# Optimization experiments

Measured on AMD Instinct MI355X. Metric: run time of the kernel, lower is better.

## Reference

```python
import jax, jax.numpy as jnp
import numpy as np

N_GOAL, N_OBS, N_TASK = 16384, 65536, 8192
E1, E2 = 1048576, 1048576
B = 256            # graphs in batch
F, S = 128, 64     # dim_features, dim_state


def setup_inputs() -> dict:
    key = jax.random.key(0)
    ks = jax.random.split(key, 16)
    inp = {
        "x_goal": jax.random.normal(ks[0], (N_GOAL, F), jnp.float32),
        "x_obs": jax.random.normal(ks[1], (N_OBS, F), jnp.float32),
        "x_task": jax.random.normal(ks[2], (N_TASK, S), jnp.float32),
        "ei_go_src": jax.random.randint(ks[3], (E1,), 0, N_GOAL),
        "ei_go_dst": jax.random.randint(ks[4], (E1,), 0, N_OBS),
        "ei_ot_src": jax.random.randint(ks[5], (E2,), 0, N_OBS),
        "ei_ot_dst": jax.random.randint(ks[6], (E2,), 0, N_TASK),
        # contiguous graph assignment: 32 task nodes per graph
        "task_batch": jnp.arange(N_TASK) // (N_TASK // B),
        # GinStandardMLP (state_gin): Lin(F,S)-ReLU-Lin(S,S)-ReLU
        "W1": jax.random.normal(ks[7], (F, S), jnp.float32) * 0.05,
        "b1": jnp.zeros((S,), jnp.float32),
        "W2": jax.random.normal(ks[8], (S, S), jnp.float32) * 0.05,
        "b2": jnp.zeros((S,), jnp.float32),
        # GinUnactivatedMLP (action_gin): Lin(S,S)-ReLU-Lin(S,1)
        "W3": jax.random.normal(ks[9], (S, S), jnp.float32) * 0.05,
        "b3": jnp.zeros((S,), jnp.float32),
        "W4": jax.random.normal(ks[10], (S, 1), jnp.float32) * 0.05,
        "b4": jnp.zeros((1,), jnp.float32),
        # critic head: Lin(2,8)-ReLU-Lin(8,1)
        "Wc1": jax.random.normal(ks[11], (2, 8), jnp.float32) * 0.5,
        "bc1": jnp.zeros((8,), jnp.float32),
        "Wc2": jax.random.normal(ks[12], (8, 1), jnp.float32) * 0.5,
        "bc2": jnp.zeros((1,), jnp.float32),
    }
    return inp


def reference(x_goal, x_obs, x_task,
              ei_go_src, ei_go_dst, ei_ot_src, ei_ot_dst, task_batch,
              W1, b1, W2, b2, W3, b3, W4, b4, Wc1, bc1, Wc2, bc2):
    # --- state_gin: GINConv((goal, obs)), eps=0 ---
    agg1 = jax.ops.segment_sum(x_goal[ei_go_src], ei_go_dst, num_segments=N_OBS)
    h = x_obs + agg1                              # (1+eps)*x_dst + sum_j x_src
    h = jax.nn.relu(h @ W1 + b1)
    x1 = jax.nn.relu(h @ W2 + b2)                 # [N_OBS, S]

    # --- action_gin: GINConv((obs, task)), eps=0 ---
    agg2 = jax.ops.segment_sum(x1[ei_ot_src], ei_ot_dst, num_segments=N_TASK)
    g = x_task + agg2
    g = jax.nn.relu(g @ W3 + b3)
    x2 = g @ W4 + b4                              # [N_TASK, 1]

    # --- critic path: global max / mean pool over task nodes per graph ---
    max_pool = jax.ops.segment_max(x2, task_batch, num_segments=B)   # [B, 1]
    cnt = jax.ops.segment_sum(jnp.ones((N_TASK, 1), x2.dtype), task_batch, num_segments=B)
    mean_pool = jax.ops.segment_sum(x2, task_batch, num_segments=B) / cnt  # [B, 1]

    pooled = jnp.concatenate([max_pool.max(axis=1, keepdims=True),
                              mean_pool.mean(axis=1, keepdims=True)], axis=1)  # [B, 2]
    out = jax.nn.relu(pooled @ Wc1 + bc1) @ Wc2 + bc2                 # [B, 1]
    return out.squeeze(-1)                                            # [B]
```

## Files before the change

### kernel.cpp

```cpp
#include <hip/hip_runtime.h>
#include <hip/hip_bf16.h>


#define CAP1 2816
#define CAP2 5120

__global__ __launch_bounds__(256) void gemm_all(
    const float* __restrict__ x_goal, const float* __restrict__ x_obs,
    const float* __restrict__ W, float* __restrict__ xg1,
    float* __restrict__ obs)
{
    __shared__ float Ws[128 * 64];
    __shared__ float Xs[16 * 132];
    const int tid = threadIdx.x;
    const float* X;
    float* O;
    int row0;
    if (blockIdx.x < 1024) { X = x_goal; O = xg1; row0 = blockIdx.x * 16; }
    else                   { X = x_obs;  O = obs; row0 = (blockIdx.x - 1024) * 16; }
    for (int i = tid; i < 128 * 64 / 4; i += 256)
        ((float4*)Ws)[i] = ((const float4*)W)[i];
    for (int i = tid; i < 16 * 32; i += 256) {
        int r = i >> 5, c4 = i & 31;
        float4 v = ((const float4*)(X + (size_t)(row0 + r) * 128))[c4];
        *((float4*)(Xs + r * 132 + c4 * 4)) = v;
    }
    __syncthreads();
    const int rl = tid >> 4;
    const int cg = (tid & 15) * 4;
    float a0 = 0.f, a1 = 0.f, a2 = 0.f, a3 = 0.f;
    const float* xr = Xs + rl * 132;
    #pragma unroll 8
    for (int k = 0; k < 128; ++k) {
        float xv = xr[k];
        float4 wv = *((const float4*)(Ws + k * 64 + cg));
        a0 = fmaf(xv, wv.x, a0);
        a1 = fmaf(xv, wv.y, a1);
        a2 = fmaf(xv, wv.z, a2);
        a3 = fmaf(xv, wv.w, a3);
    }
    float4 o; o.x = a0; o.y = a1; o.z = a2; o.w = a3;
    *((float4*)(O + (size_t)(row0 + rl) * 64 + cg)) = o;
}

__global__ __launch_bounds__(256) void bin_edges_all(
    const int* __restrict__ go_src, const int* __restrict__ go_dst,
    const int* __restrict__ ot_src, const int* __restrict__ ot_dst,
    int* __restrict__ gcur1, int* __restrict__ gcur2,
    int* __restrict__ pairs1, int* __restrict__ pairs2, int nblk1)
{
    __shared__ int hist[512];
    __shared__ int cur[512];
    const int tid = threadIdx.x;
    const bool s1 = (int)blockIdx.x < nblk1;
    const int* src = s1 ? go_src : ot_src;
    const int* dst = s1 ? go_dst : ot_dst;
    int* gcur  = s1 ? gcur1 : gcur2;
    int* pairs = s1 ? pairs1 : pairs2;
    const int bsh  = s1 ? 7 : 5;
    const int rowm = s1 ? 127 : 31;
    const int nb   = s1 ? 512 : 256;
    const int cap  = s1 ? CAP1 : CAP2;
    const int blk  = s1 ? blockIdx.x : blockIdx.x - nblk1;

    for (int i = tid; i < nb; i += 256) hist[i] = 0;
    __syncthreads();
    const int base = blk * 4096;
    const int4* d4 = (const int4*)(dst + base);
    const int4* s4 = (const int4*)(src + base);
    int4 dv[4];
    #pragma unroll
    for (int k = 0; k < 4; ++k) {
        dv[k] = d4[k * 256 + tid];
        atomicAdd(&hist[dv[k].x >> bsh], 1);
        atomicAdd(&hist[dv[k].y >> bsh], 1);
        atomicAdd(&hist[dv[k].z >> bsh], 1);
        atomicAdd(&hist[dv[k].w >> bsh], 1);
    }
    __syncthreads();
    for (int i = tid; i < nb; i += 256)
        cur[i] = atomicAdd(&gcur[i], hist[i]);
    __syncthreads();
    #pragma unroll
    for (int k = 0; k < 4; ++k) {
        int4 sv = s4[k * 256 + tid];
        int d, s, b, p;
        d = dv[k].x; s = sv.x; b = d >> bsh; p = atomicAdd(&cur[b], 1);
        if (p < cap) pairs[(size_t)b * cap + p] = ((d & rowm) << 17) | s;
        d = dv[k].y; s = sv.y; b = d >> bsh; p = atomicAdd(&cur[b], 1);
        if (p < cap) pairs[(size_t)b * cap + p] = ((d & rowm) << 17) | s;
        d = dv[k].z; s = sv.z; b = d >> bsh; p = atomicAdd(&cur[b], 1);
        if (p < cap) pairs[(size_t)b * cap + p] = ((d & rowm) << 17) | s;
        d = dv[k].w; s = sv.w; b = d >> bsh; p = atomicAdd(&cur[b], 1);
        if (p < cap) pairs[(size_t)b * cap + p] = ((d & rowm) << 17) | s;
    }
}

__global__ __launch_bounds__(1024) void gather_mlp_obs(
    const int* __restrict__ pairs, const int* __restrict__ cnt,
    const float* __restrict__ xg1, const float* __restrict__ obs,
    const float* __restrict__ b1, const float* __restrict__ W2,
    const float* __restrict__ b2, float* __restrict__ x1)
{
    constexpr int ROWS = 128;
    __shared__ int ssrc[CAP1];
    __shared__ int offs[ROWS + 1];
    __shared__ int rcnt[ROWS];
    __shared__ float W2t[64 * 68];
    __shared__ float hb[16 * 64];
    const int tid = threadIdx.x;
    const int b = blockIdx.x;

    #pragma unroll
    for (int i = tid; i < 4096; i += 1024) {
        int k = i >> 6, c = i & 63;
        W2t[c * 68 + k] = W2[i];
    }
    if (tid < ROWS) rcnt[tid] = 0;
    __syncthreads();
    int n = cnt[b];
    if (n > CAP1) n = CAP1;
    const int* bp = pairs + (size_t)b * CAP1;

    int e0 = -1, e1 = -1, e2 = -1;
    {
        int i = tid;
        if (i < n) {
            e0 = bp[i]; atomicAdd(&rcnt[e0 >> 17], 1); i += 1024;
            if (i < n) {
                e1 = bp[i]; atomicAdd(&rcnt[e1 >> 17], 1); i += 1024;
                if (i < n) { e2 = bp[i]; atomicAdd(&rcnt[e2 >> 17], 1); }
            }
        }
    }
    __syncthreads();
    if (tid < 64) {
        int v0 = rcnt[2 * tid], v1 = rcnt[2 * tid + 1];
        int s = v0 + v1;
        #pragma unroll
        for (int d = 1; d < 64; d <<= 1) {
            int t = __shfl_up(s, d);
            if (tid >= d) s += t;
        }
        int ex = s - v0 - v1;
        offs[2 * tid] = ex;
        offs[2 * tid + 1] = ex + v0;
        rcnt[2 * tid] = ex;
        rcnt[2 * tid + 1] = ex + v0;
        if (tid == 63) offs[ROWS] = s;
    }
    __syncthreads();
    if (e0 >= 0) { int p = atomicAdd(&rcnt[e0 >> 17], 1); ssrc[p] = e0 & 0x1FFFF; }
    if (e1 >= 0) { int p = atomicAdd(&rcnt[e1 >> 17], 1); ssrc[p] = e1 & 0x1FFFF; }
    if (e2 >= 0) { int p = atomicAdd(&rcnt[e2 >> 17], 1); ssrc[p] = e2 & 0x1FFFF; }
    __syncthreads();
    const int wv = tid >> 6;
    const int lane = tid & 63;
    const float bb1 = b1[lane];
    const float bb2 = b2[lane];
    float* hp = hb + wv * 64;
    const float4* h4 = (const float4*)hp;
    const float4* wrow = (const float4*)(W2t + lane * 68);
    for (int r = wv; r < ROWS; r += 16) {
        int beg = offs[r], end = offs[r + 1];
        float a0 = 0.f, a1 = 0.f, a2 = 0.f, a3 = 0.f;
        int e = beg;
        for (; e + 4 <= end; e += 4) {
            int s0 = ssrc[e], s1 = ssrc[e + 1], s2 = ssrc[e + 2], s3 = ssrc[e + 3];
            a0 += xg1[(size_t)s0 * 64 + lane];
            a1 += xg1[(size_t)s1 * 64 + lane];
            a2 += xg1[(size_t)s2 * 64 + lane];
            a3 += xg1[(size_t)s3 * 64 + lane];
        }
        for (; e < end; ++e)
            a0 += xg1[(size_t)ssrc[e] * 64 + lane];
        size_t gi = (((size_t)b * ROWS) + r) * 64 + lane;
        float acc = (a0 + a1) + (a2 + a3) + obs[gi];
        hp[lane] = fmaxf(acc + bb1, 0.f);
        float a = bb2;
        #pragma unroll 8
        for (int kc = 0; kc < 16; ++kc) {
            float4 hv = h4[kc];
            float4 wv4 = wrow[kc];
            a = fmaf(hv.x, wv4.x, a);
            a = fmaf(hv.y, wv4.y, a);
            a = fmaf(hv.z, wv4.z, a);
            a = fmaf(hv.w, wv4.w, a);
        }
        x1[gi] = fmaxf(a, 0.f);
    }
}

__global__ __launch_bounds__(1024) void gather_mlp_task_pool(
    const int* __restrict__ pairs, const int* __restrict__ cnt,
    const float* __restrict__ x1, const float* __restrict__ x_task,
    const float* __restrict__ W3, const float* __restrict__ b3,
    const float* __restrict__ W4, const float* __restrict__ b4,
    const float* __restrict__ Wc1, const float* __restrict__ bc1,
    const float* __restrict__ Wc2, const float* __restrict__ bc2,
    float* __restrict__ out)
{
    constexpr int ROWS = 32;
    __shared__ int ssrc[CAP2];
    __shared__ int offs[ROWS + 1];
    __shared__ int rcnt[ROWS];
    __shared__ float W3t[64 * 68];
    __shared__ float hb[16 * 64];
    __shared__ float xrow[ROWS];
    const int tid = threadIdx.x;
    const int b = blockIdx.x;

    #pragma unroll
    for (int i = tid; i < 4096; i += 1024) {
        int k = i >> 6, c = i & 63;
        W3t[c * 68 + k] = W3[i];
    }
    if (tid < ROWS) rcnt[tid] = 0;
    __syncthreads();
    int n = cnt[b];
    if (n > CAP2) n = CAP2;
    const int* bp = pairs + (size_t)b * CAP2;

    int e0 = -1, e1 = -1, e2 = -1, e3 = -1, e4 = -1;
    {
        int i = tid;
        if (i < n) { e0 = bp[i]; atomicAdd(&rcnt[e0 >> 17], 1); i += 1024;
        if (i < n) { e1 = bp[i]; atomicAdd(&rcnt[e1 >> 17], 1); i += 1024;
        if (i < n) { e2 = bp[i]; atomicAdd(&rcnt[e2 >> 17], 1); i += 1024;
        if (i < n) { e3 = bp[i]; atomicAdd(&rcnt[e3 >> 17], 1); i += 1024;
        if (i < n) { e4 = bp[i]; atomicAdd(&rcnt[e4 >> 17], 1); } } } } }
    }
    __syncthreads();
    if (tid < 32) {
        int v = rcnt[tid];
        int s = v;
        #pragma unroll
        for (int d = 1; d < 32; d <<= 1) {
            int t = __shfl_up(s, d);
            if (tid >= d) s += t;
        }
        int ex = s - v;
        offs[tid] = ex;
        rcnt[tid] = ex;
        if (tid == 31) offs[ROWS] = s;
    }
    __syncthreads();
    if (e0 >= 0) { int p = atomicAdd(&rcnt[e0 >> 17], 1); ssrc[p] = e0 & 0x1FFFF; }
    if (e1 >= 0) { int p = atomicAdd(&rcnt[e1 >> 17], 1); ssrc[p] = e1 & 0x1FFFF; }
    if (e2 >= 0) { int p = atomicAdd(&rcnt[e2 >> 17], 1); ssrc[p] = e2 & 0x1FFFF; }
    if (e3 >= 0) { int p = atomicAdd(&rcnt[e3 >> 17], 1); ssrc[p] = e3 & 0x1FFFF; }
    if (e4 >= 0) { int p = atomicAdd(&rcnt[e4 >> 17], 1); ssrc[p] = e4 & 0x1FFFF; }
    __syncthreads();

    const int wv = tid >> 6;
    const int lane = tid & 63;
    const float bb3 = b3[lane];
    const float w4l = W4[lane];
    const float b4c = b4[0];
    float* hp = hb + wv * 64;
    const float4* h4 = (const float4*)hp;
    const float4* wrow = (const float4*)(W3t + lane * 68);
    #pragma unroll
    for (int half = 0; half < 2; ++half) {
        const int r = wv + half * 16;
        const int row = b * ROWS + r;
        int beg = offs[r], end = offs[r + 1];
        float a0 = 0.f, a1 = 0.f, a2 = 0.f, a3 = 0.f;
        float a4 = 0.f, a5 = 0.f, a6 = 0.f, a7 = 0.f;
        int e = beg;
        for (; e + 8 <= end; e += 8) {
            int s0 = ssrc[e],     s1 = ssrc[e + 1], s2 = ssrc[e + 2], s3 = ssrc[e + 3];
            int s4 = ssrc[e + 4], s5 = ssrc[e + 5], s6 = ssrc[e + 6], s7 = ssrc[e + 7];
            a0 += x1[(size_t)s0 * 64 + lane];
            a1 += x1[(size_t)s1 * 64 + lane];
            a2 += x1[(size_t)s2 * 64 + lane];
            a3 += x1[(size_t)s3 * 64 + lane];
            a4 += x1[(size_t)s4 * 64 + lane];
            a5 += x1[(size_t)s5 * 64 + lane];
            a6 += x1[(size_t)s6 * 64 + lane];
            a7 += x1[(size_t)s7 * 64 + lane];
        }
        for (; e < end; ++e)
            a0 += x1[(size_t)ssrc[e] * 64 + lane];
        float t = ((a0 + a1) + (a2 + a3)) + ((a4 + a5) + (a6 + a7))
                + x_task[(size_t)row * 64 + lane];
        hp[lane] = t;
        float a = bb3;
        #pragma unroll 8
        for (int kc = 0; kc < 16; ++kc) {
            float4 hv = h4[kc];
            float4 wv4 = wrow[kc];
            a = fmaf(hv.x, wv4.x, a);
            a = fmaf(hv.y, wv4.y, a);
            a = fmaf(hv.z, wv4.z, a);
            a = fmaf(hv.w, wv4.w, a);
        }
        float p = fmaxf(a, 0.f) * w4l;
        p += __shfl_xor(p, 1);
        p += __shfl_xor(p, 2);
        p += __shfl_xor(p, 4);
        p += __shfl_xor(p, 8);
        p += __shfl_xor(p, 16);
        p += __shfl_xor(p, 32);
        if (lane == 0) xrow[r] = p + b4c;
    }
    __syncthreads();
    if (tid == 0) {
        float mx = -1e30f, sm = 0.f;
        #pragma unroll
        for (int i = 0; i < ROWS; ++i) {
            float v = xrow[i];
            mx = fmaxf(mx, v);
            sm += v;
        }
        float mn = sm * (1.f / 32.f);
        float o = bc2[0];
        #pragma unroll
        for (int j = 0; j < 8; ++j) {
            float t = fmaxf(mx * Wc1[j] + mn * Wc1[8 + j] + bc1[j], 0.f);
            o = fmaf(t, Wc2[j], o);
        }
        out[b] = o;
    }
}

extern "C" void kernel_launch(void* const* d_in, const int* in_sizes, int n_in,
                              void* d_out, int out_size, void* d_ws, size_t ws_size,
                              hipStream_t stream)
{
    const float* x_goal = (const float*)d_in[0];
    const float* x_obs  = (const float*)d_in[1];
    const float* x_task = (const float*)d_in[2];
    const int* go_src = (const int*)d_in[3];
    const int* go_dst = (const int*)d_in[4];
    const int* ot_src = (const int*)d_in[5];
    const int* ot_dst = (const int*)d_in[6];
    const float* W1  = (const float*)d_in[8];
    const float* b1  = (const float*)d_in[9];
    const float* W2  = (const float*)d_in[10];
    const float* b2  = (const float*)d_in[11];
    const float* W3  = (const float*)d_in[12];
    const float* b3  = (const float*)d_in[13];
    const float* W4  = (const float*)d_in[14];
    const float* b4  = (const float*)d_in[15];
    const float* Wc1 = (const float*)d_in[16];
    const float* bc1 = (const float*)d_in[17];
    const float* Wc2 = (const float*)d_in[18];
    const float* bc2 = (const float*)d_in[19];
    float* out = (float*)d_out;

    const int N_GOAL = 16384, N_OBS = 65536;
    const int E1 = in_sizes[3], E2 = in_sizes[5];
    const int NB1 = 512, NB2 = 256;

    char* w = (char*)d_ws;
    float* obs    = (float*)w;  w += (size_t)N_OBS * 64 * 4;
    float* x1     = (float*)w;  w += (size_t)N_OBS * 64 * 4;
    float* xg1    = (float*)w;  w += (size_t)N_GOAL * 64 * 4;
    int*   pairs1 = (int*)w;    w += (size_t)NB1 * CAP1 * 4;
    int*   pairs2 = (int*)w;    w += (size_t)NB2 * CAP2 * 4;
    int*   gcur1  = (int*)w;    w += NB1 * 4;
    int*   gcur2  = (int*)w;    w += NB2 * 4;

    hipMemsetAsync(gcur1, 0, (NB1 + NB2) * 4, stream);

    const int nblk1 = E1 / 4096;
    bin_edges_all<<<nblk1 + E2 / 4096, 256, 0, stream>>>(
        go_src, go_dst, ot_src, ot_dst, gcur1, gcur2, pairs1, pairs2, nblk1);
    gemm_all<<<(N_GOAL + N_OBS) / 16, 256, 0, stream>>>(x_goal, x_obs, W1, xg1, obs);
    gather_mlp_obs<<<NB1, 1024, 0, stream>>>(pairs1, gcur1, xg1, obs, b1, W2, b2, x1);
    gather_mlp_task_pool<<<NB2, 1024, 0, stream>>>(pairs2, gcur2, x1, x_task,
                                                   W3, b3, W4, b4,
                                                   Wc1, bc1, Wc2, bc2, out);
}
```

Measured before the change: 242.6 us.

## Register-tile gemm_all with 8x8 per-thread outputs and K-chunked swizzled LDS

Rewrites the first-layer projection GEMM so each block handles 256 rows and each thread computes an 8x8 output tile. K is processed in 32-wide chunks staged through LDS, with an XOR swizzle on the X tile to avoid bank conflicts. This cuts per-FMA LDS traffic and the redundant full-W reload that every 16-row block did before. In exchange it launches far fewer blocks (320 instead of 5120) and uses 64 accumulators per thread, which may lower occupancy.

Measured after the change: 242.8 us. Within noise of the previous version (+0.1%).

```diff
diff --git a/kernel.cpp b/kernel.cpp
--- a/kernel.cpp
+++ b/kernel.cpp
@@ -10,37 +10,78 @@
     const float* __restrict__ W, float* __restrict__ xg1,
     float* __restrict__ obs)
 {
-    __shared__ float Ws[128 * 64];
-    __shared__ float Xs[16 * 132];
+    __shared__ float Ws[32 * 64];
+    __shared__ float Xs[256 * 32];
     const int tid = threadIdx.x;
     const float* X;
     float* O;
     int row0;
-    if (blockIdx.x < 1024) { X = x_goal; O = xg1; row0 = blockIdx.x * 16; }
-    else                   { X = x_obs;  O = obs; row0 = (blockIdx.x - 1024) * 16; }
-    for (int i = tid; i < 128 * 64 / 4; i += 256)
-        ((float4*)Ws)[i] = ((const float4*)W)[i];
-    for (int i = tid; i < 16 * 32; i += 256) {
-        int r = i >> 5, c4 = i & 31;
-        float4 v = ((const float4*)(X + (size_t)(row0 + r) * 128))[c4];
-        *((float4*)(Xs + r * 132 + c4 * 4)) = v;
-    }
-    __syncthreads();
-    const int rl = tid >> 4;
-    const int cg = (tid & 15) * 4;
-    float a0 = 0.f, a1 = 0.f, a2 = 0.f, a3 = 0.f;
-    const float* xr = Xs + rl * 132;
-    #pragma unroll 8
-    for (int k = 0; k < 128; ++k) {
-        float xv = xr[k];
-        float4 wv = *((const float4*)(Ws + k * 64 + cg));
-        a0 = fmaf(xv, wv.x, a0);
-        a1 = fmaf(xv, wv.y, a1);
-        a2 = fmaf(xv, wv.z, a2);
-        a3 = fmaf(xv, wv.w, a3);
-    }
-    float4 o; o.x = a0; o.y = a1; o.z = a2; o.w = a3;
-    *((float4*)(O + (size_t)(row0 + rl) * 64 + cg)) = o;
+    if (blockIdx.x < 64) { X = x_goal; O = xg1; row0 = blockIdx.x * 256; }
+    else                 { X = x_obs;  O = obs; row0 = (blockIdx.x - 64) * 256; }
+    const int tcol = tid & 7;
+    const int trow = tid >> 3;
+    const int c0 = tcol * 8;
+    const int r0 = trow * 8;
+    const int swz = trow & 7;
+    float acc[8][8];
+    #pragma unroll
+    for (int i = 0; i < 8; ++i)
+        #pragma unroll
+        for (int j = 0; j < 8; ++j) acc[i][j] = 0.f;
+
+    for (int kc = 0; kc < 4; ++kc) {
+        const int k0 = kc * 32;
+        if (kc) __syncthreads();
+        #pragma unroll
+        for (int m = 0; m < 2; ++m) {
+            int i = m * 256 + tid;
+            int k = i >> 4, c4 = i & 15;
+            *(float4*)(Ws + k * 64 + c4 * 4) =
+                *(const float4*)(W + (size_t)(k0 + k) * 64 + c4 * 4);
+        }
+        #pragma unroll
+        for (int m = 0; m < 8; ++m) {
+            int kb = tid & 7;
+            int tr = tid >> 3;
+            int row = tr * 8 + m;
+            float4 v = *(const float4*)(X + (size_t)(row0 + row) * 128 + k0 + kb * 4);
+            *(float4*)(Xs + row * 32 + ((kb ^ (tr & 7)) << 2)) = v;
+        }
+        __syncthreads();
+        #pragma unroll 2
+        for (int kb = 0; kb < 8; ++kb) {
+            float4 xv[8];
+            #pragma unroll
+            for (int i = 0; i < 8; ++i)
+                xv[i] = *(const float4*)(Xs + (r0 + i) * 32 + ((kb ^ swz) << 2));
+            #pragma unroll
+            for (int kk = 0; kk < 4; ++kk) {
+                float4 w0 = *(const float4*)(Ws + (kb * 4 + kk) * 64 + c0);
+                float4 w1 = *(const float4*)(Ws + (kb * 4 + kk) * 64 + c0 + 4);
+                #pragma unroll
+                for (int i = 0; i < 8; ++i) {
+                    float xk = (kk == 0) ? xv[i].x : (kk == 1) ? xv[i].y
+                             : (kk == 2) ? xv[i].z : xv[i].w;
+                    acc[i][0] = fmaf(xk, w0.x, acc[i][0]);
+                    acc[i][1] = fmaf(xk, w0.y, acc[i][1]);
+                    acc[i][2] = fmaf(xk, w0.z, acc[i][2]);
+                    acc[i][3] = fmaf(xk, w0.w, acc[i][3]);
+                    acc[i][4] = fmaf(xk, w1.x, acc[i][4]);
+                    acc[i][5] = fmaf(xk, w1.y, acc[i][5]);
+                    acc[i][6] = fmaf(xk, w1.z, acc[i][6]);
+                    acc[i][7] = fmaf(xk, w1.w, acc[i][7]);
+                }
+            }
+        }
+    }
+    #pragma unroll
+    for (int i = 0; i < 8; ++i) {
+        float4 o0; o0.x = acc[i][0]; o0.y = acc[i][1]; o0.z = acc[i][2]; o0.w = acc[i][3];
+        float4 o1; o1.x = acc[i][4]; o1.y = acc[i][5]; o1.z = acc[i][6]; o1.w = acc[i][7];
+        float* p = O + (size_t)(row0 + r0 + i) * 64 + c0;
+        *(float4*)p = o0;
+        *(float4*)(p + 4) = o1;
+    }
 }
 
 __global__ __launch_bounds__(256) void bin_edges_all(
@@ -367,7 +408,7 @@
     const int nblk1 = E1 / 4096;
     bin_edges_all<<<nblk1 + E2 / 4096, 256, 0, stream>>>(
         go_src, go_dst, ot_src, ot_dst, gcur1, gcur2, pairs1, pairs2, nblk1);
-    gemm_all<<<(N_GOAL + N_OBS) / 16, 256, 0, stream>>>(x_goal, x_obs, W1, xg1, obs);
+    gemm_all<<<(N_GOAL + N_OBS) / 256, 256, 0, stream>>>(x_goal, x_obs, W1, xg1, obs);
     gather_mlp_obs<<<NB1, 1024, 0, stream>>>(pairs1, gcur1, xg1, obs, b1, W2, b2, x1);
     gather_mlp_task_pool<<<NB2, 1024, 0, stream>>>(pairs2, gcur2, x1, x_task,
                                                    W3, b3, W4, b4,
```

## Fuse GEMM into edge-binning kernel and keep MLP weights in registers

Applied to the files above, without the earlier changes.

Merges the input GEMM and the edge-binning pass into one launch: 256 blocks do a row-per-wave GEMM with W1 columns held in 128 registers per lane, and the remaining blocks bin edges. The small 64x64 MLP layers in both gather kernels now keep their weight column in registers and broadcast hidden activations with readlane instead of staging through shared memory. The aim is to cut a kernel launch, overlap compute-bound GEMM with atomic-heavy binning, and remove LDS traffic and syncs. In exchange, register pressure rises sharply (128-float and 64-float arrays in 256- and 1024-thread blocks), which can cause spills or lower occupancy, and the GEMM now reads x rows through uniform per-wave loads with no reuse across columns beyond the wave.

New measurement: 326.9 us. 34.7% more time.

```diff
diff --git a/kernel.cpp b/kernel.cpp
--- a/kernel.cpp
+++ b/kernel.cpp
@@ -4,95 +4,94 @@
 
 #define CAP1 2816
 #define CAP2 5120
-
-__global__ __launch_bounds__(256) void gemm_all(
+#define GEMM_BLKS 256
+
+#define RLANE(v, k) __uint_as_float(__builtin_amdgcn_readlane(__float_as_uint(v), (k)))
+
+__global__ __launch_bounds__(256) void prep(
     const float* __restrict__ x_goal, const float* __restrict__ x_obs,
     const float* __restrict__ W, float* __restrict__ xg1,
-    float* __restrict__ obs)
-{
-    __shared__ float Ws[128 * 64];
-    __shared__ float Xs[16 * 132];
-    const int tid = threadIdx.x;
-    const float* X;
-    float* O;
-    int row0;
-    if (blockIdx.x < 1024) { X = x_goal; O = xg1; row0 = blockIdx.x * 16; }
-    else                   { X = x_obs;  O = obs; row0 = (blockIdx.x - 1024) * 16; }
-    for (int i = tid; i < 128 * 64 / 4; i += 256)
-        ((float4*)Ws)[i] = ((const float4*)W)[i];
-    for (int i = tid; i < 16 * 32; i += 256) {
-        int r = i >> 5, c4 = i & 31;
-        float4 v = ((const float4*)(X + (size_t)(row0 + r) * 128))[c4];
-        *((float4*)(Xs + r * 132 + c4 * 4)) = v;
-    }
-    __syncthreads();
-    const int rl = tid >> 4;
-    const int cg = (tid & 15) * 4;
-    float a0 = 0.f, a1 = 0.f, a2 = 0.f, a3 = 0.f;
-    const float* xr = Xs + rl * 132;
-    #pragma unroll 8
-    for (int k = 0; k < 128; ++k) {
-        float xv = xr[k];
-        float4 wv = *((const float4*)(Ws + k * 64 + cg));
-        a0 = fmaf(xv, wv.x, a0);
-        a1 = fmaf(xv, wv.y, a1);
-        a2 = fmaf(xv, wv.z, a2);
-        a3 = fmaf(xv, wv.w, a3);
-    }
-    float4 o; o.x = a0; o.y = a1; o.z = a2; o.w = a3;
-    *((float4*)(O + (size_t)(row0 + rl) * 64 + cg)) = o;
-}
-
-__global__ __launch_bounds__(256) void bin_edges_all(
+    float* __restrict__ obs,
     const int* __restrict__ go_src, const int* __restrict__ go_dst,
     const int* __restrict__ ot_src, const int* __restrict__ ot_dst,
     int* __restrict__ gcur1, int* __restrict__ gcur2,
     int* __restrict__ pairs1, int* __restrict__ pairs2, int nblk1)
 {
-    __shared__ int hist[512];
-    __shared__ int cur[512];
+    __shared__ int binsmem[1024];
     const int tid = threadIdx.x;
-    const bool s1 = (int)blockIdx.x < nblk1;
-    const int* src = s1 ? go_src : ot_src;
-    const int* dst = s1 ? go_dst : ot_dst;
-    int* gcur  = s1 ? gcur1 : gcur2;
-    int* pairs = s1 ? pairs1 : pairs2;
-    const int bsh  = s1 ? 7 : 5;
-    const int rowm = s1 ? 127 : 31;
-    const int nb   = s1 ? 512 : 256;
-    const int cap  = s1 ? CAP1 : CAP2;
-    const int blk  = s1 ? blockIdx.x : blockIdx.x - nblk1;
-
-    for (int i = tid; i < nb; i += 256) hist[i] = 0;
-    __syncthreads();
-    const int base = blk * 4096;
-    const int4* d4 = (const int4*)(dst + base);
-    const int4* s4 = (const int4*)(src + base);
-    int4 dv[4];
-    #pragma unroll
-    for (int k = 0; k < 4; ++k) {
-        dv[k] = d4[k * 256 + tid];
-        atomicAdd(&hist[dv[k].x >> bsh], 1);
-        atomicAdd(&hist[dv[k].y >> bsh], 1);
-        atomicAdd(&hist[dv[k].z >> bsh], 1);
-        atomicAdd(&hist[dv[k].w >> bsh], 1);
-    }
-    __syncthreads();
-    for (int i = tid; i < nb; i += 256)
-        cur[i] = atomicAdd(&gcur[i], hist[i]);
-    __syncthreads();
-    #pragma unroll
-    for (int k = 0; k < 4; ++k) {
-        int4 sv = s4[k * 256 + tid];
-        int d, s, b, p;
-        d = dv[k].x; s = sv.x; b = d >> bsh; p = atomicAdd(&cur[b], 1);
-        if (p < cap) pairs[(size_t)b * cap + p] = ((d & rowm) << 17) | s;
-        d = dv[k].y; s = sv.y; b = d >> bsh; p = atomicAdd(&cur[b], 1);
-        if (p < cap) pairs[(size_t)b * cap + p] = ((d & rowm) << 17) | s;
-        d = dv[k].z; s = sv.z; b = d >> bsh; p = atomicAdd(&cur[b], 1);
-        if (p < cap) pairs[(size_t)b * cap + p] = ((d & rowm) << 17) | s;
-        d = dv[k].w; s = sv.w; b = d >> bsh; p = atomicAdd(&cur[b], 1);
-        if (p < cap) pairs[(size_t)b * cap + p] = ((d & rowm) << 17) | s;
+
+    if (blockIdx.x < GEMM_BLKS) {
+        const int lane = tid & 63;
+        const int gw = blockIdx.x * 4 + (tid >> 6);
+        float wreg[128];
+        #pragma unroll
+        for (int k = 0; k < 128; ++k)
+            wreg[k] = W[k * 64 + lane];
+        for (int r = gw; r < 81920; r += 1024) {
+            const int ur = __builtin_amdgcn_readfirstlane(r);
+            const float* X;
+            float* O;
+            int row;
+            if (ur < 16384) { X = x_goal; O = xg1; row = ur; }
+            else            { X = x_obs;  O = obs; row = ur - 16384; }
+            const float* xr = X + ((size_t)row << 7);
+            float q0 = 0.f, q1 = 0.f, q2 = 0.f, q3 = 0.f;
+            #pragma unroll
+            for (int k4 = 0; k4 < 32; ++k4) {
+                float4 xv = *(const float4*)(xr + (k4 << 2));
+                q0 = fmaf(xv.x, wreg[k4 * 4 + 0], q0);
+                q1 = fmaf(xv.y, wreg[k4 * 4 + 1], q1);
+                q2 = fmaf(xv.z, wreg[k4 * 4 + 2], q2);
+                q3 = fmaf(xv.w, wreg[k4 * 4 + 3], q3);
+            }
+            O[(size_t)row * 64 + lane] = (q0 + q1) + (q2 + q3);
+        }
+    } else {
+        int* hist = binsmem;
+        int* cur  = binsmem + 512;
+        const int blk2 = blockIdx.x - GEMM_BLKS;
+        const bool s1 = blk2 < nblk1;
+        const int* src = s1 ? go_src : ot_src;
+        const int* dst = s1 ? go_dst : ot_dst;
+        int* gcur  = s1 ? gcur1 : gcur2;
+        int* pairs = s1 ? pairs1 : pairs2;
+        const int bsh  = s1 ? 7 : 5;
+        const int rowm = s1 ? 127 : 31;
+        const int nb   = s1 ? 512 : 256;
+        const int cap  = s1 ? CAP1 : CAP2;
+        const int blk  = s1 ? blk2 : blk2 - nblk1;
+
+        for (int i = tid; i < nb; i += 256) hist[i] = 0;
+        __syncthreads();
+        const int base = blk * 4096;
+        const int4* d4 = (const int4*)(dst + base);
+        const int4* s4 = (const int4*)(src + base);
+        int4 dv[4];
+        #pragma unroll
+        for (int k = 0; k < 4; ++k) {
+            dv[k] = d4[k * 256 + tid];
+            atomicAdd(&hist[dv[k].x >> bsh], 1);
+            atomicAdd(&hist[dv[k].y >> bsh], 1);
+            atomicAdd(&hist[dv[k].z >> bsh], 1);
+            atomicAdd(&hist[dv[k].w >> bsh], 1);
+        }
+        __syncthreads();
+        for (int i = tid; i < nb; i += 256)
+            cur[i] = atomicAdd(&gcur[i], hist[i]);
+        __syncthreads();
+        #pragma unroll
+        for (int k = 0; k < 4; ++k) {
+            int4 sv = s4[k * 256 + tid];
+            int d, s, b, p;
+            d = dv[k].x; s = sv.x; b = d >> bsh; p = atomicAdd(&cur[b], 1);
+            if (p < cap) pairs[(size_t)b * cap + p] = ((d & rowm) << 17) | s;
+            d = dv[k].y; s = sv.y; b = d >> bsh; p = atomicAdd(&cur[b], 1);
+            if (p < cap) pairs[(size_t)b * cap + p] = ((d & rowm) << 17) | s;
+            d = dv[k].z; s = sv.z; b = d >> bsh; p = atomicAdd(&cur[b], 1);
+            if (p < cap) pairs[(size_t)b * cap + p] = ((d & rowm) << 17) | s;
+            d = dv[k].w; s = sv.w; b = d >> bsh; p = atomicAdd(&cur[b], 1);
+            if (p < cap) pairs[(size_t)b * cap + p] = ((d & rowm) << 17) | s;
+        }
     }
 }
 
@@ -106,16 +105,15 @@
     __shared__ int ssrc[CAP1];
     __shared__ int offs[ROWS + 1];
     __shared__ int rcnt[ROWS];
-    __shared__ float W2t[64 * 68];
-    __shared__ float hb[16 * 64];
     const int tid = threadIdx.x;
+    const int lane = tid & 63;
     const int b = blockIdx.x;
 
+    float wreg[64];
     #pragma unroll
-    for (int i = tid; i < 4096; i += 1024) {
-        int k = i >> 6, c = i & 63;
-        W2t[c * 68 + k] = W2[i];
-    }
+    for (int k = 0; k < 64; ++k)
+        wreg[k] = W2[k * 64 + lane];
+
     if (tid < ROWS) rcnt[tid] = 0;
     __syncthreads();
     int n = cnt[b];
@@ -155,12 +153,8 @@
     if (e2 >= 0) { int p = atomicAdd(&rcnt[e2 >> 17], 1); ssrc[p] = e2 & 0x1FFFF; }
     __syncthreads();
     const int wv = tid >> 6;
-    const int lane = tid & 63;
     const float bb1 = b1[lane];
     const float bb2 = b2[lane];
-    float* hp = hb + wv * 64;
-    const float4* h4 = (const float4*)hp;
-    const float4* wrow = (const float4*)(W2t + lane * 68);
     for (int r = wv; r < ROWS; r += 16) {
         int beg = offs[r], end = offs[r + 1];
         float a0 = 0.f, a1 = 0.f, a2 = 0.f, a3 = 0.f;
@@ -175,19 +169,16 @@
         for (; e < end; ++e)
             a0 += xg1[(size_t)ssrc[e] * 64 + lane];
         size_t gi = (((size_t)b * ROWS) + r) * 64 + lane;
-        float acc = (a0 + a1) + (a2 + a3) + obs[gi];
-        hp[lane] = fmaxf(acc + bb1, 0.f);
-        float a = bb2;
-        #pragma unroll 8
-        for (int kc = 0; kc < 16; ++kc) {
-            float4 hv = h4[kc];
-            float4 wv4 = wrow[kc];
-            a = fmaf(hv.x, wv4.x, a);
-            a = fmaf(hv.y, wv4.y, a);
-            a = fmaf(hv.z, wv4.z, a);
-            a = fmaf(hv.w, wv4.w, a);
-        }
-        x1[gi] = fmaxf(a, 0.f);
+        float h = fmaxf((a0 + a1) + (a2 + a3) + obs[gi] + bb1, 0.f);
+        float q0 = bb2, q1 = 0.f, q2 = 0.f, q3 = 0.f;
+        #pragma unroll
+        for (int k = 0; k < 64; k += 4) {
+            q0 = fmaf(RLANE(h, k),     wreg[k],     q0);
+            q1 = fmaf(RLANE(h, k + 1), wreg[k + 1], q1);
+            q2 = fmaf(RLANE(h, k + 2), wreg[k + 2], q2);
+            q3 = fmaf(RLANE(h, k + 3), wreg[k + 3], q3);
+        }
+        x1[gi] = fmaxf((q0 + q1) + (q2 + q3), 0.f);
     }
 }
 
@@ -204,17 +195,16 @@
     __shared__ int ssrc[CAP2];
     __shared__ int offs[ROWS + 1];
     __shared__ int rcnt[ROWS];
-    __shared__ float W3t[64 * 68];
-    __shared__ float hb[16 * 64];
     __shared__ float xrow[ROWS];
     const int tid = threadIdx.x;
+    const int lane = tid & 63;
     const int b = blockIdx.x;
 
+    float wreg[64];
     #pragma unroll
-    for (int i = tid; i < 4096; i += 1024) {
-        int k = i >> 6, c = i & 63;
-        W3t[c * 68 + k] = W3[i];
-    }
+    for (int k = 0; k < 64; ++k)
+        wreg[k] = W3[k * 64 + lane];
+
     if (tid < ROWS) rcnt[tid] = 0;
     __syncthreads();
     int n = cnt[b];
@@ -253,13 +243,9 @@
     __syncthreads();
 
     const int wv = tid >> 6;
-    const int lane = tid & 63;
     const float bb3 = b3[lane];
     const float w4l = W4[lane];
     const float b4c = b4[0];
-    float* hp = hb + wv * 64;
-    const float4* h4 = (const float4*)hp;
-    const float4* wrow = (const float4*)(W3t + lane * 68);
     #pragma unroll
     for (int half = 0; half < 2; ++half) {
         const int r = wv + half * 16;
@@ -284,18 +270,15 @@
             a0 += x1[(size_t)ssrc[e] * 64 + lane];
         float t = ((a0 + a1) + (a2 + a3)) + ((a4 + a5) + (a6 + a7))
                 + x_task[(size_t)row * 64 + lane];
-        hp[lane] = t;
-        float a = bb3;
-        #pragma unroll 8
-        for (int kc = 0; kc < 16; ++kc) {
-            float4 hv = h4[kc];
-            float4 wv4 = wrow[kc];
-            a = fmaf(hv.x, wv4.x, a);
-            a = fmaf(hv.y, wv4.y, a);
-            a = fmaf(hv.z, wv4.z, a);
-            a = fmaf(hv.w, wv4.w, a);
-        }
-        float p = fmaxf(a, 0.f) * w4l;
+        float q0 = bb3, q1 = 0.f, q2 = 0.f, q3 = 0.f;
+        #pragma unroll
+        for (int k = 0; k < 64; k += 4) {
+            q0 = fmaf(RLANE(t, k),     wreg[k],     q0);
+            q1 = fmaf(RLANE(t, k + 1), wreg[k + 1], q1);
+            q2 = fmaf(RLANE(t, k + 2), wreg[k + 2], q2);
+            q3 = fmaf(RLANE(t, k + 3), wreg[k + 3], q3);
+        }
+        float p = fmaxf((q0 + q1) + (q2 + q3), 0.f) * w4l;
         p += __shfl_xor(p, 1);
         p += __shfl_xor(p, 2);
         p += __shfl_xor(p, 4);
@@ -349,7 +332,7 @@
     const float* bc2 = (const float*)d_in[19];
     float* out = (float*)d_out;
 
-    const int N_GOAL = 16384, N_OBS = 65536;
+    const int N_OBS = 65536, N_GOAL = 16384;
     const int E1 = in_sizes[3], E2 = in_sizes[5];
     const int NB1 = 512, NB2 = 256;
 
@@ -365,9 +348,10 @@
     hipMemsetAsync(gcur1, 0, (NB1 + NB2) * 4, stream);
 
     const int nblk1 = E1 / 4096;
-    bin_edges_all<<<nblk1 + E2 / 4096, 256, 0, stream>>>(
+    const int nblk2 = E2 / 4096;
+    prep<<<GEMM_BLKS + nblk1 + nblk2, 256, 0, stream>>>(
+        x_goal, x_obs, W1, xg1, obs,
         go_src, go_dst, ot_src, ot_dst, gcur1, gcur2, pairs1, pairs2, nblk1);
-    gemm_all<<<(N_GOAL + N_OBS) / 16, 256, 0, stream>>>(x_goal, x_obs, W1, xg1, obs);
     gather_mlp_obs<<<NB1, 1024, 0, stream>>>(pairs1, gcur1, xg1, obs, b1, W2, b2, x1);
     gather_mlp_task_pool<<<NB2, 1024, 0, stream>>>(pairs2, gcur2, x1, x_task,
                                                    W3, b3, W4, b4,
```

## Fuse W1 GEMM into edge-binning kernel with register-resident weights and readlane broadcast

Applied to the files above, without the earlier changes.

Merges the separate x@W1 GEMM and edge-binning kernels into one launch. The first 256 blocks run the GEMM and the remaining blocks run the existing binning, so the two independent stages can overlap and one launch disappears. The GEMM is rewritten so each wavefront keeps one column of W1 in 128 registers and processes 80 rows, two at a time. Each row's inputs are broadcast with readlane instead of going through shared memory, and the next row pair is prefetched. This cuts the LDS traffic and the per-block reload of W1, but adds heavy register pressure and a long serial chain of scalar readlane operations per wavefront.

New measurement: 276.7 us. 1.14x slower.

```diff
diff --git a/kernel.cpp b/kernel.cpp
--- a/kernel.cpp
+++ b/kernel.cpp
@@ -4,95 +4,116 @@
 
 #define CAP1 2816
 #define CAP2 5120
-
-__global__ __launch_bounds__(256) void gemm_all(
+#define GEMM_BLKS 256
+
+#define RLANE(v, k) __uint_as_float(__builtin_amdgcn_readlane(__float_as_uint(v), (k)))
+
+__global__ __launch_bounds__(256, 2) void prep(
     const float* __restrict__ x_goal, const float* __restrict__ x_obs,
-    const float* __restrict__ W, float* __restrict__ xg1,
-    float* __restrict__ obs)
-{
-    __shared__ float Ws[128 * 64];
-    __shared__ float Xs[16 * 132];
-    const int tid = threadIdx.x;
-    const float* X;
-    float* O;
-    int row0;
-    if (blockIdx.x < 1024) { X = x_goal; O = xg1; row0 = blockIdx.x * 16; }
-    else                   { X = x_obs;  O = obs; row0 = (blockIdx.x - 1024) * 16; }
-    for (int i = tid; i < 128 * 64 / 4; i += 256)
-        ((float4*)Ws)[i] = ((const float4*)W)[i];
-    for (int i = tid; i < 16 * 32; i += 256) {
-        int r = i >> 5, c4 = i & 31;
-        float4 v = ((const float4*)(X + (size_t)(row0 + r) * 128))[c4];
-        *((float4*)(Xs + r * 132 + c4 * 4)) = v;
-    }
-    __syncthreads();
-    const int rl = tid >> 4;
-    const int cg = (tid & 15) * 4;
-    float a0 = 0.f, a1 = 0.f, a2 = 0.f, a3 = 0.f;
-    const float* xr = Xs + rl * 132;
-    #pragma unroll 8
-    for (int k = 0; k < 128; ++k) {
-        float xv = xr[k];
-        float4 wv = *((const float4*)(Ws + k * 64 + cg));
-        a0 = fmaf(xv, wv.x, a0);
-        a1 = fmaf(xv, wv.y, a1);
-        a2 = fmaf(xv, wv.z, a2);
-        a3 = fmaf(xv, wv.w, a3);
-    }
-    float4 o; o.x = a0; o.y = a1; o.z = a2; o.w = a3;
-    *((float4*)(O + (size_t)(row0 + rl) * 64 + cg)) = o;
-}
-
-__global__ __launch_bounds__(256) void bin_edges_all(
+    const float* W, float* __restrict__ xg1, float* __restrict__ obs,
     const int* __restrict__ go_src, const int* __restrict__ go_dst,
     const int* __restrict__ ot_src, const int* __restrict__ ot_dst,
     int* __restrict__ gcur1, int* __restrict__ gcur2,
     int* __restrict__ pairs1, int* __restrict__ pairs2, int nblk1)
 {
-    __shared__ int hist[512];
-    __shared__ int cur[512];
+    __shared__ int binsmem[1024];
     const int tid = threadIdx.x;
-    const bool s1 = (int)blockIdx.x < nblk1;
-    const int* src = s1 ? go_src : ot_src;
-    const int* dst = s1 ? go_dst : ot_dst;
-    int* gcur  = s1 ? gcur1 : gcur2;
-    int* pairs = s1 ? pairs1 : pairs2;
-    const int bsh  = s1 ? 7 : 5;
-    const int rowm = s1 ? 127 : 31;
-    const int nb   = s1 ? 512 : 256;
-    const int cap  = s1 ? CAP1 : CAP2;
-    const int blk  = s1 ? blockIdx.x : blockIdx.x - nblk1;
-
-    for (int i = tid; i < nb; i += 256) hist[i] = 0;
-    __syncthreads();
-    const int base = blk * 4096;
-    const int4* d4 = (const int4*)(dst + base);
-    const int4* s4 = (const int4*)(src + base);
-    int4 dv[4];
-    #pragma unroll
-    for (int k = 0; k < 4; ++k) {
-        dv[k] = d4[k * 256 + tid];
-        atomicAdd(&hist[dv[k].x >> bsh], 1);
-        atomicAdd(&hist[dv[k].y >> bsh], 1);
-        atomicAdd(&hist[dv[k].z >> bsh], 1);
-        atomicAdd(&hist[dv[k].w >> bsh], 1);
-    }
-    __syncthreads();
-    for (int i = tid; i < nb; i += 256)
-        cur[i] = atomicAdd(&gcur[i], hist[i]);
-    __syncthreads();
-    #pragma unroll
-    for (int k = 0; k < 4; ++k) {
-        int4 sv = s4[k * 256 + tid];
-        int d, s, b, p;
-        d = dv[k].x; s = sv.x; b = d >> bsh; p = atomicAdd(&cur[b], 1);
-        if (p < cap) pairs[(size_t)b * cap + p] = ((d & rowm) << 17) | s;
-        d = dv[k].y; s = sv.y; b = d >> bsh; p = atomicAdd(&cur[b], 1);
-        if (p < cap) pairs[(size_t)b * cap + p] = ((d & rowm) << 17) | s;
-        d = dv[k].z; s = sv.z; b = d >> bsh; p = atomicAdd(&cur[b], 1);
-        if (p < cap) pairs[(size_t)b * cap + p] = ((d & rowm) << 17) | s;
-        d = dv[k].w; s = sv.w; b = d >> bsh; p = atomicAdd(&cur[b], 1);
-        if (p < cap) pairs[(size_t)b * cap + p] = ((d & rowm) << 17) | s;
+
+    if (blockIdx.x < GEMM_BLKS) {
+        const int lane = tid & 63;
+        const int q = lane & 31;
+        const int gw = blockIdx.x * 4 + (tid >> 6);
+        const int rbase = gw * 80;
+
+        float wreg[128];
+        #pragma unroll
+        for (int k = 0; k < 128; ++k)
+            wreg[k] = W[k * 64 + lane];
+
+        float4 xv;
+        {
+            int r = rbase + ((lane >> 5) & 1);
+            const float* p = (r < 16384) ? x_goal + ((size_t)r << 7)
+                                         : x_obs + ((size_t)(r - 16384) << 7);
+            xv = *(const float4*)(p + (q << 2));
+        }
+        for (int pi = 0; pi < 40; ++pi) {
+            const int rA = rbase + 2 * pi;
+            const int rB = rA + 1;
+            float4 nxt;
+            if (pi < 39) {
+                int r = rA + 2 + ((lane >> 5) & 1);
+                const float* p = (r < 16384) ? x_goal + ((size_t)r << 7)
+                                             : x_obs + ((size_t)(r - 16384) << 7);
+                nxt = *(const float4*)(p + (q << 2));
+            }
+            float qa0 = 0.f, qa1 = 0.f, qa2 = 0.f, qa3 = 0.f;
+            float qb0 = 0.f, qb1 = 0.f, qb2 = 0.f, qb3 = 0.f;
+            #pragma unroll
+            for (int k4 = 0; k4 < 32; ++k4) {
+                qa0 = fmaf(RLANE(xv.x, k4), wreg[4 * k4 + 0], qa0);
+                qa1 = fmaf(RLANE(xv.y, k4), wreg[4 * k4 + 1], qa1);
+                qa2 = fmaf(RLANE(xv.z, k4), wreg[4 * k4 + 2], qa2);
+                qa3 = fmaf(RLANE(xv.w, k4), wreg[4 * k4 + 3], qa3);
+                qb0 = fmaf(RLANE(xv.x, 32 + k4), wreg[4 * k4 + 0], qb0);
+                qb1 = fmaf(RLANE(xv.y, 32 + k4), wreg[4 * k4 + 1], qb1);
+                qb2 = fmaf(RLANE(xv.z, 32 + k4), wreg[4 * k4 + 2], qb2);
+                qb3 = fmaf(RLANE(xv.w, 32 + k4), wreg[4 * k4 + 3], qb3);
+            }
+            float* oA = (rA < 16384) ? xg1 + ((size_t)rA << 6)
+                                     : obs + ((size_t)(rA - 16384) << 6);
+            float* oB = (rB < 16384) ? xg1 + ((size_t)rB << 6)
+                                     : obs + ((size_t)(rB - 16384) << 6);
+            oA[lane] = (qa0 + qa1) + (qa2 + qa3);
+            oB[lane] = (qb0 + qb1) + (qb2 + qb3);
+            if (pi < 39) xv = nxt;
+        }
+    } else {
+        int* hist = binsmem;
+        int* cur  = binsmem + 512;
+        const int blk2 = blockIdx.x - GEMM_BLKS;
+        const bool s1 = blk2 < nblk1;
+        const int* src = s1 ? go_src : ot_src;
+        const int* dst = s1 ? go_dst : ot_dst;
+        int* gcur  = s1 ? gcur1 : gcur2;
+        int* pairs = s1 ? pairs1 : pairs2;
+        const int bsh  = s1 ? 7 : 5;
+        const int rowm = s1 ? 127 : 31;
+        const int nb   = s1 ? 512 : 256;
+        const int cap  = s1 ? CAP1 : CAP2;
+        const int blk  = s1 ? blk2 : blk2 - nblk1;
+
+        for (int i = tid; i < nb; i += 256) hist[i] = 0;
+        __syncthreads();
+        const int base = blk * 4096;
+        const int4* d4 = (const int4*)(dst + base);
+        const int4* s4 = (const int4*)(src + base);
+        int4 dv[4];
+        #pragma unroll
+        for (int k = 0; k < 4; ++k) {
+            dv[k] = d4[k * 256 + tid];
+            atomicAdd(&hist[dv[k].x >> bsh], 1);
+            atomicAdd(&hist[dv[k].y >> bsh], 1);
+            atomicAdd(&hist[dv[k].z >> bsh], 1);
+            atomicAdd(&hist[dv[k].w >> bsh], 1);
+        }
+        __syncthreads();
+        for (int i = tid; i < nb; i += 256)
+            cur[i] = atomicAdd(&gcur[i], hist[i]);
+        __syncthreads();
+        #pragma unroll
+        for (int k = 0; k < 4; ++k) {
+            int4 sv = s4[k * 256 + tid];
+            int d, s, b, p;
+            d = dv[k].x; s = sv.x; b = d >> bsh; p = atomicAdd(&cur[b], 1);
+            if (p < cap) pairs[(size_t)b * cap + p] = ((d & rowm) << 17) | s;
+            d = dv[k].y; s = sv.y; b = d >> bsh; p = atomicAdd(&cur[b], 1);
+            if (p < cap) pairs[(size_t)b * cap + p] = ((d & rowm) << 17) | s;
+            d = dv[k].z; s = sv.z; b = d >> bsh; p = atomicAdd(&cur[b], 1);
+            if (p < cap) pairs[(size_t)b * cap + p] = ((d & rowm) << 17) | s;
+            d = dv[k].w; s = sv.w; b = d >> bsh; p = atomicAdd(&cur[b], 1);
+            if (p < cap) pairs[(size_t)b * cap + p] = ((d & rowm) << 17) | s;
+        }
     }
 }
 
@@ -349,7 +370,7 @@
     const float* bc2 = (const float*)d_in[19];
     float* out = (float*)d_out;
 
-    const int N_GOAL = 16384, N_OBS = 65536;
+    const int N_OBS = 65536, N_GOAL = 16384;
     const int E1 = in_sizes[3], E2 = in_sizes[5];
     const int NB1 = 512, NB2 = 256;
 
@@ -365,9 +386,10 @@
     hipMemsetAsync(gcur1, 0, (NB1 + NB2) * 4, stream);
 
     const int nblk1 = E1 / 4096;
-    bin_edges_all<<<nblk1 + E2 / 4096, 256, 0, stream>>>(
+    const int nblk2 = E2 / 4096;
+    prep<<<GEMM_BLKS + nblk1 + nblk2, 256, 0, stream>>>(
+        x_goal, x_obs, W1, xg1, obs,
         go_src, go_dst, ot_src, ot_dst, gcur1, gcur2, pairs1, pairs2, nblk1);
-    gemm_all<<<(N_GOAL + N_OBS) / 16, 256, 0, stream>>>(x_goal, x_obs, W1, xg1, obs);
     gather_mlp_obs<<<NB1, 1024, 0, stream>>>(pairs1, gcur1, xg1, obs, b1, W2, b2, x1);
     gather_mlp_task_pool<<<NB2, 1024, 0, stream>>>(pairs2, gcur2, x1, x_task,
                                                    W3, b3, W4, b4,
```
